# Performance work log

Hardware: AMD Instinct MI355X
Metric: run time of the kernel (lower is better)

## Reference

```python
import jax, jax.numpy as jnp
import numpy as np

D_MODEL = 1024
N_HEADS = 16
HEAD_DIM = D_MODEL // N_HEADS
B, S = 2, 2048


def setup_inputs() -> dict:
    key = jax.random.key(0)
    ks = jax.random.split(key, 12)
    sd = 1.0 / np.sqrt(D_MODEL)
    inp = {
        "x": jax.random.normal(ks[0], (B, S, D_MODEL), dtype=jnp.float32),
        "rel_bias": jax.random.normal(ks[1], (N_HEADS, S, S), dtype=jnp.float32) * 0.02,
        "attn_mask": jnp.zeros((1, 1, S, S), dtype=jnp.float32),
        # Linear params in torch layout: W [out, in], b [out]
        "Wq": jax.random.normal(ks[2], (D_MODEL, D_MODEL), dtype=jnp.float32) * sd,
        "bq": jnp.zeros((D_MODEL,), dtype=jnp.float32),
        "Wk": jax.random.normal(ks[3], (D_MODEL, D_MODEL), dtype=jnp.float32) * sd,
        "bk": jnp.zeros((D_MODEL,), dtype=jnp.float32),
        "Wv": jax.random.normal(ks[4], (D_MODEL, D_MODEL), dtype=jnp.float32) * sd,
        "bv": jnp.zeros((D_MODEL,), dtype=jnp.float32),
        "Wo": jax.random.normal(ks[5], (D_MODEL, D_MODEL), dtype=jnp.float32) * sd,
        "bo": jnp.zeros((D_MODEL,), dtype=jnp.float32),
    }
    return inp


def _split_heads(t):
    # [B, S, D] -> [B, H, S, Hd]
    b, s, _ = t.shape
    return t.reshape(b, s, N_HEADS, HEAD_DIM).transpose(0, 2, 1, 3)


def reference(x, rel_bias, attn_mask, Wq, bq, Wk, bk, Wv, bv, Wo, bo):
    scale = HEAD_DIM ** (-0.5)
    q = _split_heads(x @ Wq.T + bq)  # [B, H, S, Hd]
    k = _split_heads(x @ Wk.T + bk)
    v = _split_heads(x @ Wv.T + bv)
    scores = jnp.einsum("bhqd,bhkd->bhqk", q, k) * scale
    scores = scores + rel_bias  # [H,S,S] broadcasts over batch
    scores = scores + attn_mask  # [1,1,S,S]
    probs = jax.nn.softmax(scores, axis=-1)
    ctx = jnp.einsum("bhqk,bhkd->bhqd", probs, v)  # [B, H, S, Hd]
    ctx = ctx.transpose(0, 2, 1, 3).reshape(x.shape[0], x.shape[1], D_MODEL)
    return ctx @ Wo.T + bo
```

## Files before the change

kernel.cpp:

```cpp
#include <hip/hip_runtime.h>
#include <hip/hip_bf16.h>
#include <stdint.h>

#define S_LEN 2048
#define DM 1024
#define NH 16
#define HD 64

typedef __bf16 bf16x8 __attribute__((ext_vector_type(8)));
typedef float f32x4 __attribute__((ext_vector_type(4)));
typedef unsigned short u16x4 __attribute__((ext_vector_type(4)));

#if __has_builtin(__builtin_amdgcn_exp2f)
#define EXP2F(x) __builtin_amdgcn_exp2f(x)
#else
#define EXP2F(x) exp2f(x)
#endif

__device__ __forceinline__ unsigned short f2bf(float f){
  union { float f; uint32_t u; } v; v.f = f;
  uint32_t r = v.u + 0x7fffu + ((v.u >> 16) & 1u);
  return (unsigned short)(r >> 16);
}

__device__ __forceinline__ float bf2f(unsigned short u){
  union { uint32_t u; float f; } v; v.u = ((uint32_t)u) << 16;
  return v.f;
}

__device__ __forceinline__ void load_lds16(const void* g, void* l){
  __builtin_amdgcn_global_load_lds((const __attribute__((address_space(1))) void*)g,
                                   (__attribute__((address_space(3))) void*)l, 16, 0, 0);
}

__device__ __forceinline__ f32x4 mfma16(bf16x8 a, bf16x8 b, f32x4 c){
  return __builtin_amdgcn_mfma_f32_16x16x32_bf16(a, b, c, 0, 0, 0);
}

__device__ __forceinline__ bf16x8 lds_swz_read(const unsigned short* base, int row, int cb){
  int addr = (row << 7) + (cb ^ ((row & 7) << 4));
  return *reinterpret_cast<const bf16x8*>(reinterpret_cast<const char*>(base) + addr);
}

__global__ void prep_kernel(const float* __restrict__ x,
                            const float* __restrict__ wq, const float* __restrict__ wk,
                            const float* __restrict__ wv, const float* __restrict__ wo,
                            unsigned short* __restrict__ ws_base){
  long idx = ((long)blockIdx.x * 256 + threadIdx.x) * 4;
  const float* s; unsigned short* d; long off;
  if (idx < (1L << 22)) { s = x; d = ws_base; off = idx; }
  else {
    long r = idx - (1L << 22);
    int wsel = (int)(r >> 20);
    off = r & ((1L << 20) - 1);
    s = wsel == 0 ? wq : wsel == 1 ? wk : wsel == 2 ? wv : wo;
    d = ws_base + (1L << 22) + ((long)wsel << 20);
  }
  float4 f = *reinterpret_cast<const float4*>(s + off);
  u16x4 o;
  o[0] = f2bf(f.x); o[1] = f2bf(f.y); o[2] = f2bf(f.z); o[3] = f2bf(f.w);
  *reinterpret_cast<u16x4*>(d + off) = o;
}

template<int MODE>
__global__ __launch_bounds__(256, 2)
void gemm_bt_kernel(const unsigned short* __restrict__ A,
                    const unsigned short* __restrict__ B0,
                    const unsigned short* __restrict__ B1,
                    const unsigned short* __restrict__ B2,
                    const float* __restrict__ bias0,
                    const float* __restrict__ bias1,
                    const float* __restrict__ bias2,
                    unsigned short* __restrict__ q_out,
                    unsigned short* __restrict__ k_out,
                    unsigned short* __restrict__ vt_out,
                    float* __restrict__ f_out)
{
  __shared__ unsigned short As[128 * 64];
  __shared__ unsigned short Bs[128 * 64];
  const int tid = threadIdx.x;
  const int lane = tid & 63;
  const int w = tid >> 6;
  const int wr = w >> 1, wc = w & 1;
  const int mBase = blockIdx.y * 128;
  int nb = blockIdx.x;
  const unsigned short* Bmat; const float* bias; int mat;
  if constexpr (MODE == 0) {
    mat = nb >> 3;
    nb &= 7;
    Bmat = mat == 0 ? B0 : (mat == 1 ? B1 : B2);
    bias = mat == 0 ? bias0 : (mat == 1 ? bias1 : bias2);
  } else { mat = 0; Bmat = B0; bias = bias0; }
  const int nBase = nb * 128;

  f32x4 acc[4][4] = {};
  const int srow = lane >> 3;
  const int ksrc = ((lane & 7) ^ srow) * 8;
  const unsigned short* ArowBase = A    + (size_t)(mBase + w * 32 + srow) * DM + ksrc;
  const unsigned short* BrowBase = Bmat + (size_t)(nBase + w * 32 + srow) * DM + ksrc;

  for (int kt = 0; kt < 16; ++kt) {
    #pragma unroll
    for (int i = 0; i < 4; ++i) {
      load_lds16(ArowBase + (size_t)(i * 8) * DM + kt * 64, &As[(w * 4 + i) * 512]);
      load_lds16(BrowBase + (size_t)(i * 8) * DM + kt * 64, &Bs[(w * 4 + i) * 512]);
    }
    __syncthreads();
    #pragma unroll
    for (int kk = 0; kk < 2; ++kk) {
      bf16x8 af[4], bfr[4];
      const int cb = kk * 64 + ((lane >> 4) << 4);
      #pragma unroll
      for (int m = 0; m < 4; ++m)
        af[m] = lds_swz_read(As, wr * 64 + m * 16 + (lane & 15), cb);
      #pragma unroll
      for (int n = 0; n < 4; ++n)
        bfr[n] = lds_swz_read(Bs, wc * 64 + n * 16 + (lane & 15), cb);
      #pragma unroll
      for (int m = 0; m < 4; ++m)
        #pragma unroll
        for (int n = 0; n < 4; ++n)
          acc[m][n] = mfma16(af[m], bfr[n], acc[m][n]);
    }
    __syncthreads();
  }

  #pragma unroll
  for (int m = 0; m < 4; ++m) {
    #pragma unroll
    for (int n = 0; n < 4; ++n) {
      const int col = nBase + wc * 64 + n * 16 + (lane & 15);
      const float bv = bias[col];
      const int row0 = mBase + wr * 64 + m * 16 + ((lane >> 4) << 2);
      if constexpr (MODE == 1) {
        #pragma unroll
        for (int j = 0; j < 4; ++j)
          f_out[(size_t)(row0 + j) * DM + col] = acc[m][n][j] + bv;
      } else {
        const int h = col >> 6, d = col & 63;
        if (mat < 2) {
          unsigned short* dst = (mat == 0) ? q_out : k_out;
          #pragma unroll
          for (int j = 0; j < 4; ++j) {
            const int row = row0 + j;
            const int b = row >> 11, s = row & 2047;
            dst[(((size_t)b * NH + h) * S_LEN + s) * HD + d] = f2bf(acc[m][n][j] + bv);
          }
        } else {
          const int b = row0 >> 11, s = row0 & 2047;
          u16x4 pk;
          #pragma unroll
          for (int j = 0; j < 4; ++j) pk[j] = f2bf(acc[m][n][j] + bv);
          *reinterpret_cast<u16x4*>(&vt_out[(((size_t)b * NH + h) * HD + d) * S_LEN + s]) = pk;
        }
      }
    }
  }
}


#define WAITV8 do { asm volatile("s_waitcnt vmcnt(8)" ::: "memory"); } while (0)
#define WAITV4 do { asm volatile("s_waitcnt vmcnt(4)" ::: "memory"); } while (0)
#define WAITV0 do { asm volatile("s_waitcnt vmcnt(0)" ::: "memory"); } while (0)
#define SB0    __builtin_amdgcn_sched_barrier(0)
#define BAR    __builtin_amdgcn_s_barrier()

#define LOAD_RAW(lB) do {                                                     \
    rb0 = *reinterpret_cast<const f32x4*>(bp + (lB) + g * 4);                 \
    rm0 = *reinterpret_cast<const f32x4*>(mp + (lB) + g * 4);                 \
    rb1 = *reinterpret_cast<const f32x4*>(bp + (lB) + 16 + g * 4);            \
    rm1 = *reinterpret_cast<const f32x4*>(mp + (lB) + 16 + g * 4);            \
    rb2 = *reinterpret_cast<const f32x4*>(bp + (lB) + 32 + g * 4);            \
    rm2 = *reinterpret_cast<const f32x4*>(mp + (lB) + 32 + g * 4);            \
    rb3 = *reinterpret_cast<const f32x4*>(bp + (lB) + 48 + g * 4);            \
    rm3 = *reinterpret_cast<const f32x4*>(mp + (lB) + 48 + g * 4);            \
  } while (0)

#define COMBINE do {                                                          \
    bm0 = (rb0 + rm0) * L2E; bm1 = (rb1 + rm1) * L2E;                         \
    bm2 = (rb2 + rm2) * L2E; bm3 = (rb3 + rm3) * L2E;                         \
  } while (0)

#define STAGE_K(kvB) do {                                                                    \
    load_lds16(Kp + (size_t)((kvB) + w * 16 + srow) * HD + ksrc,     &Ks[(w * 2) * 512]);    \
    load_lds16(Kp + (size_t)((kvB) + w * 16 + 8 + srow) * HD + ksrc, &Ks[(w * 2 + 1) * 512]);\
  } while (0)

#define STAGE_V(kvB) do {                                                                    \
    load_lds16(Vp + (size_t)(w * 16 + srow) * S_LEN + (kvB) + ksrc,     &Vs[(w * 2) * 512]);    \
    load_lds16(Vp + (size_t)(w * 16 + 8 + srow) * S_LEN + (kvB) + ksrc, &Vs[(w * 2 + 1) * 512]);\
  } while (0)

#define BIAS_COL(SCN, BMN) do {                                               \
    SCN[0] = SCN[0] * SC + BMN[0];                                            \
    SCN[1] = SCN[1] * SC + BMN[1];                                            \
    SCN[2] = SCN[2] * SC + BMN[2];                                            \
    SCN[3] = SCN[3] * SC + BMN[3];                                            \
    mt_ = fmaxf(mt_, fmaxf(fmaxf(SCN[0], SCN[1]), fmaxf(SCN[2], SCN[3])));    \
  } while (0)

#define EXP_COL(SCN) do {                                                     \
    SCN[0] = EXP2F(SCN[0] - mn_); SCN[1] = EXP2F(SCN[1] - mn_);               \
    SCN[2] = EXP2F(SCN[2] - mn_); SCN[3] = EXP2F(SCN[3] - mn_);               \
  } while (0)

#define PWR_COL(NN, SCN) do {                                                 \
    u16x4 pk_;                                                                \
    pk_[0] = f2bf(SCN[0]); pk_[1] = f2bf(SCN[1]);                             \
    pk_[2] = f2bf(SCN[2]); pk_[3] = f2bf(SCN[3]);                             \
    const int colb_ = ((NN) * 16 + 4 * g) * 2;                                \
    *reinterpret_cast<u16x4*>(                                                \
        reinterpret_cast<char*>(Pw_) + (q << 7) + (colb_ ^ ((q & 7) << 4))) = pk_; \
  } while (0)

#define COMPUTE_TILE do {                                                     \
    f32x4 sc0_, sc1_, sc2_, sc3_;                                             \
    { bf16x8 a_ = lds_swz_read(Ks, 0 * 16 + q, cbq);                          \
      bf16x8 b_ = lds_swz_read(Ks, 0 * 16 + q, 64 + cbq);                     \
      f32x4 z_ = {}; z_ = mfma16(a_, qf0, z_); sc0_ = mfma16(b_, qf1, z_); }  \
    { bf16x8 a_ = lds_swz_read(Ks, 1 * 16 + q, cbq);                          \
      bf16x8 b_ = lds_swz_read(Ks, 1 * 16 + q, 64 + cbq);                     \
      f32x4 z_ = {}; z_ = mfma16(a_, qf0, z_); sc1_ = mfma16(b_, qf1, z_); }  \
    { bf16x8 a_ = lds_swz_read(Ks, 2 * 16 + q, cbq);                          \
      bf16x8 b_ = lds_swz_read(Ks, 2 * 16 + q, 64 + cbq);                     \
      f32x4 z_ = {}; z_ = mfma16(a_, qf0, z_); sc2_ = mfma16(b_, qf1, z_); }  \
    { bf16x8 a_ = lds_swz_read(Ks, 3 * 16 + q, cbq);                          \
      bf16x8 b_ = lds_swz_read(Ks, 3 * 16 + q, 64 + cbq);                     \
      f32x4 z_ = {}; z_ = mfma16(a_, qf0, z_); sc3_ = mfma16(b_, qf1, z_); }  \
    float mt_ = -3.0e38f;                                                     \
    BIAS_COL(sc0_, bm0); BIAS_COL(sc1_, bm1);                                 \
    BIAS_COL(sc2_, bm2); BIAS_COL(sc3_, bm3);                                 \
    mt_ = fmaxf(mt_, __shfl_xor(mt_, 16));                                    \
    mt_ = fmaxf(mt_, __shfl_xor(mt_, 32));                                    \
    const float mn_ = fmaxf(m_run, mt_);                                      \
    const float corr_ = EXP2F(m_run - mn_);                                   \
    m_run = mn_;                                                              \
    EXP_COL(sc0_); EXP_COL(sc1_); EXP_COL(sc2_); EXP_COL(sc3_);               \
    f32x4 ls4_ = sc0_ + sc1_ + sc2_ + sc3_;                                   \
    float ls_ = ls4_[0] + ls4_[1] + ls4_[2] + ls4_[3];                        \
    ls_ += __shfl_xor(ls_, 16);                                               \
    ls_ += __shfl_xor(ls_, 32);                                               \
    l_run = l_run * corr_ + ls_;                                              \
    acc0_ *= corr_; acc1_ *= corr_; acc2_ *= corr_; acc3_ *= corr_;           \
    PWR_COL(0, sc0_); PWR_COL(1, sc1_); PWR_COL(2, sc2_); PWR_COL(3, sc3_);   \
    bf16x8 pf0_ = lds_swz_read(Pw_, q, cbq);                                  \
    bf16x8 pf1_ = lds_swz_read(Pw_, q, 64 + cbq);                             \
    { bf16x8 a_ = lds_swz_read(Vs, 0 * 16 + q, cbq);                          \
      bf16x8 b_ = lds_swz_read(Vs, 0 * 16 + q, 64 + cbq);                     \
      acc0_ = mfma16(a_, pf0_, acc0_); acc0_ = mfma16(b_, pf1_, acc0_); }     \
    { bf16x8 a_ = lds_swz_read(Vs, 1 * 16 + q, cbq);                          \
      bf16x8 b_ = lds_swz_read(Vs, 1 * 16 + q, 64 + cbq);                     \
      acc1_ = mfma16(a_, pf0_, acc1_); acc1_ = mfma16(b_, pf1_, acc1_); }     \
    { bf16x8 a_ = lds_swz_read(Vs, 2 * 16 + q, cbq);                          \
      bf16x8 b_ = lds_swz_read(Vs, 2 * 16 + q, 64 + cbq);                     \
      acc2_ = mfma16(a_, pf0_, acc2_); acc2_ = mfma16(b_, pf1_, acc2_); }     \
    { bf16x8 a_ = lds_swz_read(Vs, 3 * 16 + q, cbq);                          \
      bf16x8 b_ = lds_swz_read(Vs, 3 * 16 + q, 64 + cbq);                     \
      acc3_ = mfma16(a_, pf0_, acc3_); acc3_ = mfma16(b_, pf1_, acc3_); }     \
  } while (0)

__global__ __launch_bounds__(256) __attribute__((amdgpu_waves_per_eu(4, 5)))
void attn_kernel(const unsigned short* __restrict__ Q,
                 const unsigned short* __restrict__ Kmat,
                 const unsigned short* __restrict__ Vt,
                 const float* __restrict__ rel_bias,
                 const float* __restrict__ mask,
                 unsigned short* __restrict__ ctxp0,
                 unsigned short* __restrict__ ctxp1,
                 unsigned short* __restrict__ ctxp2,
                 unsigned short* __restrict__ ctxp3,
                 float* __restrict__ Mbuf,
                 float* __restrict__ Lbuf)
{
  __shared__ unsigned short Ks[64 * 64];
  __shared__ unsigned short Vs[64 * 64];
  __shared__ unsigned short Ps[4][16 * 64];

  const int logical = (blockIdx.x & 7) * 512 + (blockIdx.x >> 3);
  const int s  = logical & 3;
  const int b  = (logical >> 2) & 1;
  const int qt = (logical >> 3) & 31;
  const int h  = logical >> 8;

  const int lane = threadIdx.x & 63, w = threadIdx.x >> 6;
  const int q = lane & 15, g = lane >> 4;
  const int bh = b * NH + h;
  const int qRow = qt * 64 + w * 16;
  const int kv0 = s << 9;
  const unsigned short* Qp = Q + ((size_t)bh * S_LEN + qRow) * HD;
  bf16x8 qf0 = *reinterpret_cast<const bf16x8*>(Qp + (size_t)q * HD + g * 8);
  bf16x8 qf1 = *reinterpret_cast<const bf16x8*>(Qp + (size_t)q * HD + 32 + g * 8);

  const unsigned short* Kp = Kmat + (size_t)bh * S_LEN * HD;
  const unsigned short* Vp = Vt + (size_t)bh * HD * S_LEN;
  const float* bp = rel_bias + (size_t)h * S_LEN * S_LEN + (size_t)(qRow + q) * S_LEN + kv0;
  const float* mp = mask + (size_t)(qRow + q) * S_LEN + kv0;

  float m_run = -3.0e38f, l_run = 0.f;
  f32x4 acc0_ = {}, acc1_ = {}, acc2_ = {}, acc3_ = {};
  f32x4 rb0, rb1, rb2, rb3, rm0, rm1, rm2, rm3;
  f32x4 bm0, bm1, bm2, bm3;

  const float SC  = 0.125f * 1.44269504089f;
  const float L2E = 1.44269504089f;

  const int srow = lane >> 3;
  const int ksrc = ((lane & 7) ^ srow) * 8;
  const int cbq = g << 4;
  unsigned short* Pw_ = Ps[w];

  LOAD_RAW(0);
  SB0;

  for (int t = 0; t < 7; ++t) {
    const int kvB = kv0 + t * 64;
    BAR;
    STAGE_K(kvB); STAGE_V(kvB);
    SB0;
    WAITV4; SB0;
    COMBINE;
    LOAD_RAW((t + 1) * 64);
    SB0;
    WAITV8; SB0;
    BAR;
    COMPUTE_TILE;
  }
  {
    const int kvB = kv0 + 7 * 64;
    BAR;
    STAGE_K(kvB); STAGE_V(kvB);
    SB0;
    WAITV4; SB0;
    COMBINE;
    WAITV0; SB0;
    BAR;
    COMPUTE_TILE;
  }

  const float inv = 1.0f / l_run;
  acc0_ *= inv; acc1_ *= inv; acc2_ *= inv; acc3_ *= inv;
  PWR_COL(0, acc0_); PWR_COL(1, acc1_); PWR_COL(2, acc2_); PWR_COL(3, acc3_);
  bf16x8 c0 = lds_swz_read(Pw_, q, g << 4);
  bf16x8 c1 = lds_swz_read(Pw_, q, 64 + (g << 4));
  unsigned short* pbase = (s == 0) ? ctxp0 : (s == 1) ? ctxp1 : (s == 2) ? ctxp2 : ctxp3;
  unsigned short* cp = pbase + ((size_t)(b * S_LEN + qRow + q)) * DM + h * HD;
  *reinterpret_cast<bf16x8*>(cp + 8 * g) = c0;
  *reinterpret_cast<bf16x8*>(cp + 32 + 8 * g) = c1;
  if (g == 0) {
    const int mlIdx = (s << 16) + (bh << 11) + qRow + q;
    Mbuf[mlIdx] = m_run;
    Lbuf[mlIdx] = l_run;
  }
}

__global__ void merge_kernel(const unsigned short* __restrict__ ctxp0,
                             const unsigned short* __restrict__ ctxp1,
                             const unsigned short* __restrict__ ctxp2,
                             const unsigned short* __restrict__ ctxp3,
                             const float* __restrict__ Mbuf,
                             const float* __restrict__ Lbuf,
                             unsigned short* __restrict__ ctx){
  const long e = ((long)blockIdx.x * 256 + threadIdx.x) * 4;
  const int b = (int)(e >> 21);
  const int srow = (int)((e >> 10) & 2047);
  const int d = (int)(e & 1023);
  const int h = d >> 6;
  const int idx = ((b * NH + h) << 11) + srow;
  const float m0 = Mbuf[idx],               m1 = Mbuf[(1 << 16) + idx];
  const float m2 = Mbuf[(2 << 16) + idx],   m3 = Mbuf[(3 << 16) + idx];
  const float l0 = Lbuf[idx],               l1 = Lbuf[(1 << 16) + idx];
  const float l2 = Lbuf[(2 << 16) + idx],   l3 = Lbuf[(3 << 16) + idx];
  const float mm = fmaxf(fmaxf(m0, m1), fmaxf(m2, m3));
  const float w0 = EXP2F(m0 - mm) * l0;
  const float w1 = EXP2F(m1 - mm) * l1;
  const float w2 = EXP2F(m2 - mm) * l2;
  const float w3 = EXP2F(m3 - mm) * l3;
  const float inv = 1.0f / (w0 + w1 + w2 + w3);
  u16x4 c0 = *reinterpret_cast<const u16x4*>(ctxp0 + e);
  u16x4 c1 = *reinterpret_cast<const u16x4*>(ctxp1 + e);
  u16x4 c2 = *reinterpret_cast<const u16x4*>(ctxp2 + e);
  u16x4 c3 = *reinterpret_cast<const u16x4*>(ctxp3 + e);
  u16x4 o;
  #pragma unroll
  for (int j = 0; j < 4; ++j)
    o[j] = f2bf((bf2f(c0[j]) * w0 + bf2f(c1[j]) * w1 +
                 bf2f(c2[j]) * w2 + bf2f(c3[j]) * w3) * inv);
  *reinterpret_cast<u16x4*>(ctx + e) = o;
}

extern "C" void kernel_launch(void* const* d_in, const int* in_sizes, int n_in,
                              void* d_out, int out_size, void* d_ws, size_t ws_size,
                              hipStream_t stream) {
  (void)in_sizes; (void)n_in; (void)out_size; (void)ws_size;
  const float* x  = (const float*)d_in[0];
  const float* rb = (const float*)d_in[1];
  const float* mk = (const float*)d_in[2];
  const float* Wq = (const float*)d_in[3];
  const float* bq = (const float*)d_in[4];
  const float* Wk = (const float*)d_in[5];
  const float* bk = (const float*)d_in[6];
  const float* Wv = (const float*)d_in[7];
  const float* bv = (const float*)d_in[8];
  const float* Wo = (const float*)d_in[9];
  const float* bo = (const float*)d_in[10];
  float* out = (float*)d_out;

  unsigned short* ws  = (unsigned short*)d_ws;
  unsigned short* xb  = ws;
  unsigned short* wqb = ws + (1L << 22);
  unsigned short* wkb = wqb + (1L << 20);
  unsigned short* wvb = wkb + (1L << 20);
  unsigned short* wob = wvb + (1L << 20);
  unsigned short* Qw  = wob + (1L << 20);
  unsigned short* Kw  = Qw + (1L << 22);
  unsigned short* Vtw = Kw + (1L << 22);
  unsigned short* ctx = Vtw + (1L << 22);
  unsigned short* ctxp1 = xb;
  unsigned short* ctxp2 = (unsigned short*)d_out;
  unsigned short* ctxp3 = (unsigned short*)d_out + (1L << 22);
  float* Mb = (float*)wqb;
  float* Lb = (float*)(wqb + (1L << 19));

  prep_kernel<<<8192, 256, 0, stream>>>(x, Wq, Wk, Wv, Wo, ws);
  gemm_bt_kernel<0><<<dim3(24, 32), 256, 0, stream>>>(
      xb, wqb, wkb, wvb, bq, bk, bv, Qw, Kw, Vtw, nullptr);
  attn_kernel<<<4096, 256, 0, stream>>>(Qw, Kw, Vtw, rb, mk, ctx, ctxp1, ctxp2, ctxp3, Mb, Lb);
  merge_kernel<<<4096, 256, 0, stream>>>(ctx, ctxp1, ctxp2, ctxp3, Mb, Lb, ctx);
  gemm_bt_kernel<1><<<dim3(8, 32), 256, 0, stream>>>(
      ctx, wob, nullptr, nullptr, bo, nullptr, nullptr, nullptr, nullptr, nullptr, out);
}
```

Measured before the change: 233.9 us.

## Prefetch K/V tiles into registers one iteration ahead instead of direct LDS loads

Replaces the direct global-to-LDS staging of K and V tiles with register prefetch. Each tile is loaded into VGPRs one iteration ahead and written to LDS at the start of the next iteration, and the vmcnt/lgkmcnt waits are reordered to match. The aim is to hide K/V global latency behind the previous tile's compute rather than waiting on it inside the same iteration. In exchange it adds VGPR pressure and extra LDS write instructions, and the hand-tuned waitcnt counts must stay correct. The write side stores at lane*8 with no swizzle, so it relies on the global read addresses already carrying the XOR swizzle.

```diff
diff --git a/kernel.cpp b/kernel.cpp
--- a/kernel.cpp
+++ b/kernel.cpp
@@ -162,6 +162,7 @@
 #define WAITV8 do { asm volatile("s_waitcnt vmcnt(8)" ::: "memory"); } while (0)
 #define WAITV4 do { asm volatile("s_waitcnt vmcnt(4)" ::: "memory"); } while (0)
 #define WAITV0 do { asm volatile("s_waitcnt vmcnt(0)" ::: "memory"); } while (0)
+#define WAITLG do { asm volatile("s_waitcnt lgkmcnt(0)" ::: "memory"); } while (0)
 #define SB0    __builtin_amdgcn_sched_barrier(0)
 #define BAR    __builtin_amdgcn_s_barrier()
 
@@ -181,14 +182,18 @@
     bm2 = (rb2 + rm2) * L2E; bm3 = (rb3 + rm3) * L2E;                         \
   } while (0)
 
-#define STAGE_K(kvB) do {                                                                    \
-    load_lds16(Kp + (size_t)((kvB) + w * 16 + srow) * HD + ksrc,     &Ks[(w * 2) * 512]);    \
-    load_lds16(Kp + (size_t)((kvB) + w * 16 + 8 + srow) * HD + ksrc, &Ks[(w * 2 + 1) * 512]);\
-  } while (0)
-
-#define STAGE_V(kvB) do {                                                                    \
-    load_lds16(Vp + (size_t)(w * 16 + srow) * S_LEN + (kvB) + ksrc,     &Vs[(w * 2) * 512]);    \
-    load_lds16(Vp + (size_t)(w * 16 + 8 + srow) * S_LEN + (kvB) + ksrc, &Vs[(w * 2 + 1) * 512]);\
+#define LOAD_KV_REG(kvB) do {                                                        \
+    kr0 = *reinterpret_cast<const bf16x8*>(Kp + (size_t)((kvB) + w * 16 + srow) * HD + ksrc);     \
+    kr1 = *reinterpret_cast<const bf16x8*>(Kp + (size_t)((kvB) + w * 16 + 8 + srow) * HD + ksrc); \
+    vr0 = *reinterpret_cast<const bf16x8*>(Vp + (size_t)(w * 16 + srow) * S_LEN + (kvB) + ksrc);  \
+    vr1 = *reinterpret_cast<const bf16x8*>(Vp + (size_t)(w * 16 + 8 + srow) * S_LEN + (kvB) + ksrc); \
+  } while (0)
+
+#define WRITE_KV_LDS do {                                                     \
+    *reinterpret_cast<bf16x8*>(&Ks[(w * 2) * 512] + lane * 8)     = kr0;      \
+    *reinterpret_cast<bf16x8*>(&Ks[(w * 2 + 1) * 512] + lane * 8) = kr1;      \
+    *reinterpret_cast<bf16x8*>(&Vs[(w * 2) * 512] + lane * 8)     = vr0;      \
+    *reinterpret_cast<bf16x8*>(&Vs[(w * 2 + 1) * 512] + lane * 8) = vr1;      \
   } while (0)
 
 #define BIAS_COL(SCN, BMN) do {                                               \
@@ -300,6 +305,7 @@
   f32x4 acc0_ = {}, acc1_ = {}, acc2_ = {}, acc3_ = {};
   f32x4 rb0, rb1, rb2, rb3, rm0, rm1, rm2, rm3;
   f32x4 bm0, bm1, bm2, bm3;
+  bf16x8 kr0, kr1, vr0, vr1;
 
   const float SC  = 0.125f * 1.44269504089f;
   const float L2E = 1.44269504089f;
@@ -309,30 +315,32 @@
   const int cbq = g << 4;
   unsigned short* Pw_ = Ps[w];
 
+  LOAD_KV_REG(kv0);
+  SB0;
   LOAD_RAW(0);
   SB0;
 
   for (int t = 0; t < 7; ++t) {
-    const int kvB = kv0 + t * 64;
     BAR;
-    STAGE_K(kvB); STAGE_V(kvB);
+    WAITV8; SB0;
+    WRITE_KV_LDS;
+    LOAD_KV_REG(kv0 + (t + 1) * 64);
     SB0;
     WAITV4; SB0;
     COMBINE;
     LOAD_RAW((t + 1) * 64);
     SB0;
-    WAITV8; SB0;
+    WAITLG; SB0;
     BAR;
     COMPUTE_TILE;
   }
   {
-    const int kvB = kv0 + 7 * 64;
     BAR;
-    STAGE_K(kvB); STAGE_V(kvB);
-    SB0;
-    WAITV4; SB0;
+    WAITV8; SB0;
+    WRITE_KV_LDS;
+    WAITV0; SB0;
     COMBINE;
-    WAITV0; SB0;
+    WAITLG; SB0;
     BAR;
     COMPUTE_TILE;
   }
```

Result: slower. 285.8 us (+22.2%).
